# Performance work log

Hardware: AMD Instinct MI355X
Metric: run time of the kernel (lower is better)

The kernel has to match this reference:

```python
import jax, jax.numpy as jnp
import numpy as np

H = 64  # LSTM hidden size (from LSTM(64, ...))

def _lstm(xs, W, U, b, return_sequences):
    """Keras-convention LSTM. xs: [B, T, D]; W: [D, 4H]; U: [H, 4H]; b: [4H].
    Gate order i, f, g(candidate), o; sigmoid recurrent activation, tanh activation."""
    B = xs.shape[0]
    h_dim = U.shape[0]
    # Precompute input projection for all timesteps (hoists the big GEMM out of scan)
    xW = jnp.einsum('btd,dk->btk', xs, W) + b  # [B, T, 4H]

    def step(carry, xw_t):
        h, c = carry
        z = xw_t + h @ U  # [B, 4H]
        i, f, g, o = jnp.split(z, 4, axis=-1)
        i = jax.nn.sigmoid(i)
        f = jax.nn.sigmoid(f)
        g = jnp.tanh(g)
        o = jax.nn.sigmoid(o)
        c = f * c + i * g
        h = o * jnp.tanh(c)
        return (h, c), h

    h0 = jnp.zeros((B, h_dim), xs.dtype)
    (hT, _), hs = jax.lax.scan(step, (h0, h0), jnp.swapaxes(xW, 0, 1))
    if return_sequences:
        return jnp.swapaxes(hs, 0, 1)  # [B, T, H]
    return hT  # [B, H]


def setup_inputs() -> dict:
    key = jax.random.key(0)
    ks = jax.random.split(key, 17)
    T = 16384
    num_actions = 10
    s = lambda *sh: 1.0 / np.sqrt(sh[0])
    d = {}
    d['x'] = jax.random.normal(ks[0], (T, 2), dtype=jnp.float32)
    # LSTM 1: input dim 2 -> 64
    d['W1'] = jax.random.normal(ks[1], (2, 4 * H), jnp.float32) * s(2)
    d['U1'] = jax.random.normal(ks[2], (H, 4 * H), jnp.float32) * s(H)
    d['b1'] = jnp.concatenate([jnp.zeros(H), jnp.ones(H), jnp.zeros(2 * H)]).astype(jnp.float32)  # unit forget bias
    # LSTM 2: 64 -> 64
    d['W2'] = jax.random.normal(ks[3], (H, 4 * H), jnp.float32) * s(H)
    d['U2'] = jax.random.normal(ks[4], (H, 4 * H), jnp.float32) * s(H)
    d['b2'] = jnp.concatenate([jnp.zeros(H), jnp.ones(H), jnp.zeros(2 * H)]).astype(jnp.float32)
    # LSTM 3: 64 -> 64 (last step only)
    d['W3'] = jax.random.normal(ks[5], (H, 4 * H), jnp.float32) * s(H)
    d['U3'] = jax.random.normal(ks[6], (H, 4 * H), jnp.float32) * s(H)
    d['b3'] = jnp.concatenate([jnp.zeros(H), jnp.ones(H), jnp.zeros(2 * H)]).astype(jnp.float32)
    # Dense heads
    d['Wd1'] = jax.random.normal(ks[7], (H, 20), jnp.float32) * s(H)
    d['bd1'] = jnp.zeros((20,), jnp.float32)
    d['Wd2'] = jax.random.normal(ks[8], (20, 20), jnp.float32) * s(20)
    d['bd2'] = jnp.zeros((20,), jnp.float32)
    d['Wl'] = jax.random.normal(ks[9], (20, num_actions), jnp.float32) * s(20)
    d['bl'] = jnp.zeros((num_actions,), jnp.float32)
    return d


def reference(x, W1, U1, b1, W2, U2, b2, W3, U3, b3, Wd1, bd1, Wd2, bd2, Wl, bl):
    # call(): reshape to [1, -1, 2], cast float32
    xs = jnp.reshape(x.astype(jnp.float32), (1, -1, 2))
    h1 = _lstm(xs, W1, U1, b1, return_sequences=True)   # [1, T, 64]
    h2 = _lstm(h1, W2, U2, b2, return_sequences=True)   # [1, T, 64]
    h3 = _lstm(h2, W3, U3, b3, return_sequences=False)  # [1, 64]
    # Dropout layers are identity at inference (no training=True in call())
    h4 = jax.nn.relu(h3 @ Wd1 + bd1)
    h6 = jax.nn.relu(h4 @ Wd2 + bd2)
    logits = h6 @ Wl + bl  # [1, num_actions]
    return logits
```

## Files before the change

kernel.cpp:

```cpp
#include <hip/hip_runtime.h>

#define H 64
#define G4 256
#define CS 512
#define NC 32
#define PB 16
#define TPB (CS / PB)
#define LOG2E 1.44269504088896f

typedef _Float16 f16x8 __attribute__((ext_vector_type(8)));
typedef float f32x4 __attribute__((ext_vector_type(4)));
typedef __fp16 p16x2 __attribute__((ext_vector_type(2)));

union I4F { int4 i; f16x8 h; };

__device__ __forceinline__ int pack_f16s(float lo, float hi, float sc) {
  union { p16x2 h; int i; } u;
  u.h = __builtin_amdgcn_cvt_pkrtz(lo * sc, hi * sc);
  return u.i;
}
__device__ __forceinline__ void wg_barrier() {
  asm volatile("s_waitcnt lgkmcnt(0)\n\ts_barrier" ::: "memory");
}

__global__ __launch_bounds__(G4) void proj_x(const float* __restrict__ x,
                                             const float* __restrict__ W,
                                             const float* __restrict__ b,
                                             float* __restrict__ xw) {
  const int t = blockIdx.x;
  const int j = threadIdx.x;
  const int G = j >> 6, u = j & 63;
  const float sc = (G == 2) ? 2.f * LOG2E : -LOG2E;
  xw[(size_t)t * G4 + u * 4 + G] =
      sc * fmaf(x[2 * t], W[j], fmaf(x[2 * t + 1], W[G4 + j], b[j]));
}

__global__ __attribute__((amdgpu_flat_work_group_size(G4, G4),
                          amdgpu_waves_per_eu(1, 1)))
void pipe_step(int q, const float* __restrict__ xw1,
               const float* __restrict__ U1, const float* __restrict__ U2,
               const float* __restrict__ U3, const float* __restrict__ W2,
               const float* __restrict__ W3, const float* __restrict__ b2,
               const float* __restrict__ b3, __fp16* __restrict__ h1s,
               __fp16* __restrict__ h2s, __fp16* __restrict__ hb3,
               float* __restrict__ xw2s, float* __restrict__ xw3s,
               float* __restrict__ cst, float* __restrict__ h3out, int T) {
  const int bid = (int)blockIdx.x;
  const int tid = (int)threadIdx.x;

  if (bid >= 3) {
    const int p = bid - 3;
    const int lay = p / PB;
    const int pb = p % PB;
    const int chunk = q - 1 - 2 * lay;
    if (chunk < 0 || chunk >= NC) return;
    const __fp16* hsrc = lay ? h2s : h1s;
    const float* Wm = lay ? W3 : W2;
    const float* bb = lay ? b3 : b2;
    float* dst = (lay ? xw3s : xw2s) + (size_t)(chunk & 1) * CS * G4;
    const int tl0 = pb * TPB;

    __shared__ float sh[TPB * H];
    {
      union { int4 i; __fp16 hh[8]; } uu;
      uu.i = ((const int4*)(hsrc + (size_t)(chunk * CS + tl0) * H))[tid];
      float4 lo = make_float4(uu.hh[0], uu.hh[1], uu.hh[2], uu.hh[3]);
      float4 hi = make_float4(uu.hh[4], uu.hh[5], uu.hh[6], uu.hh[7]);
      ((float4*)sh)[2 * tid] = lo;
      ((float4*)sh)[2 * tid + 1] = hi;
    }
    __syncthreads();

    const int j = tid;
    const int G = j >> 6, u = j & 63;
    const int pos = (u << 2) | G;
    const float scl = (G == 2) ? 2.f * LOG2E : -LOG2E;
    float w[H];
#pragma unroll
    for (int k = 0; k < H; ++k) w[k] = Wm[k * G4 + j];
    const float bj = bb[j];

    for (int tt = 0; tt < TPB; ++tt) {
      const float4* h4 = (const float4*)(sh + tt * H);
      float a0 = bj, a1 = 0.f, a2 = 0.f, a3 = 0.f;
#pragma unroll
      for (int kk = 0; kk < H / 4; ++kk) {
        float4 hv = h4[kk];
        a0 = fmaf(hv.x, w[4 * kk + 0], a0);
        a1 = fmaf(hv.y, w[4 * kk + 1], a1);
        a2 = fmaf(hv.z, w[4 * kk + 2], a2);
        a3 = fmaf(hv.w, w[4 * kk + 3], a3);
      }
      dst[(size_t)(tl0 + tt) * G4 + pos] = scl * ((a0 + a1) + (a2 + a3));
    }
    return;
  }

  const int role = bid;
  const int chunk = q - 2 * role;
  if (chunk < 0 || chunk >= NC) return;
  const int t0 = chunk * CS, t1 = t0 + CS;

  __shared__ int4 sh_h[2][8];

  const int wv = tid >> 6;
  const int n = tid & 15;
  const int kg = (tid & 63) >> 4;
  const int u_own = (wv << 4) | ((n & 3) << 2) | kg;

  const float* U = (role == 0) ? U1 : ((role == 1) ? U2 : U3);
  const float scl = ((n & 3) == 2) ? 2.f * LOG2E : -LOG2E;

  I4F au[4][2];
#pragma unroll
  for (int tau = 0; tau < 4; ++tau) {
    const int colA = ((n & 3) << 6) | (wv << 4) | (tau << 2) | (n >> 2);
#pragma unroll
    for (int kap = 0; kap < 2; ++kap) {
      const int k0 = kap * 32 + kg * 8;
      au[tau][kap].i = make_int4(
          pack_f16s(U[(k0 + 0) * G4 + colA], U[(k0 + 1) * G4 + colA], scl),
          pack_f16s(U[(k0 + 2) * G4 + colA], U[(k0 + 3) * G4 + colA], scl),
          pack_f16s(U[(k0 + 4) * G4 + colA], U[(k0 + 5) * G4 + colA], scl),
          pack_f16s(U[(k0 + 6) * G4 + colA], U[(k0 + 7) * G4 + colA], scl));
      asm volatile("" : "+v"(au[tau][kap].i.x), "+v"(au[tau][kap].i.y),
                       "+v"(au[tau][kap].i.z), "+v"(au[tau][kap].i.w));
    }
  }

  const float* xbase =
      (role == 0) ? (xw1 + (size_t)t0 * G4)
                  : ((role == 1) ? xw2s : xw3s) + (size_t)(chunk & 1) * CS * G4;
  __fp16* hout = (role == 0) ? h1s : h2s;

  float c = (chunk == 0) ? 0.f : cst[role * 64 + u_own];
  if (tid < 8) {
    int4 v = make_int4(0, 0, 0, 0);
    if (chunk > 0) {
      const int4* src = (role == 0)
              ? (const int4*)(h1s + (size_t)(t0 - 1) * H)
              : (role == 1) ? (const int4*)(h2s + (size_t)(t0 - 1) * H)
                            : (const int4*)hb3;
      v = src[tid];
    }
    sh_h[(t0 - 1) & 1][tid] = v;
  }
  wg_barrier();

  float4 nxt = *(const float4*)(xbase + (size_t)0 * G4 + u_own * 4);

  for (int tt = 0; tt < CS; ++tt) {
    const int s = t0 + tt;
    I4F b0, b1;
    b0.i = sh_h[(s - 1) & 1][kg];
    b1.i = sh_h[(s - 1) & 1][4 + kg];

    f32x4 a0 = {0.f, 0.f, 0.f, 0.f}, a1 = a0, a2 = a0, a3 = a0;
    a0 = __builtin_amdgcn_mfma_f32_16x16x32_f16(au[0][0].h, b0.h, a0, 0, 0, 0);
    a1 = __builtin_amdgcn_mfma_f32_16x16x32_f16(au[1][0].h, b0.h, a1, 0, 0, 0);
    a2 = __builtin_amdgcn_mfma_f32_16x16x32_f16(au[2][0].h, b0.h, a2, 0, 0, 0);
    a3 = __builtin_amdgcn_mfma_f32_16x16x32_f16(au[3][0].h, b0.h, a3, 0, 0, 0);
    a0 = __builtin_amdgcn_mfma_f32_16x16x32_f16(au[0][1].h, b1.h, a0, 0, 0, 0);
    a1 = __builtin_amdgcn_mfma_f32_16x16x32_f16(au[1][1].h, b1.h, a1, 0, 0, 0);
    a2 = __builtin_amdgcn_mfma_f32_16x16x32_f16(au[2][1].h, b1.h, a2, 0, 0, 0);
    a3 = __builtin_amdgcn_mfma_f32_16x16x32_f16(au[3][1].h, b1.h, a3, 0, 0, 0);

    const bool se = ((n & 1) == 0);
    const bool s01 = ((n & 2) == 0);
    float z0, z1, z2, z3;
    {
      float lo, hi;
      lo = se ? a0[0] : a1[0]; hi = se ? a2[0] : a3[0]; z0 = s01 ? lo : hi;
      lo = se ? a0[1] : a1[1]; hi = se ? a2[1] : a3[1]; z1 = s01 ? lo : hi;
      lo = se ? a0[2] : a1[2]; hi = se ? a2[2] : a3[2]; z2 = s01 ? lo : hi;
      lo = se ? a0[3] : a1[3]; hi = se ? a2[3] : a3[3]; z3 = s01 ? lo : hi;
    }
    z0 += nxt.x; z1 += nxt.y; z2 += nxt.z; z3 += nxt.w;

    const int tn = (tt + 1 < CS) ? (tt + 1) : tt;
    nxt = *(const float4*)(xbase + (size_t)tn * G4 + u_own * 4);

    const float gi = __builtin_amdgcn_rcpf(1.f + exp2f(z0));
    const float gf = __builtin_amdgcn_rcpf(1.f + exp2f(z1));
    const float gg = fmaf(-2.f, __builtin_amdgcn_rcpf(1.f + exp2f(z2)), 1.f);
    const float go = __builtin_amdgcn_rcpf(1.f + exp2f(z3));
    c = fmaf(gf, c, gi * gg);
    const float th =
        fmaf(-2.f, __builtin_amdgcn_rcpf(1.f + exp2f(c * (2.f * LOG2E))), 1.f);
    const float h = go * th;

    if (n < 4) {
      ((__fp16*)&sh_h[s & 1][0])[u_own] = (__fp16)h;
      if (role < 2) {
        hout[(size_t)s * H + u_own] = (__fp16)h;
      } else {
        if (tt == CS - 1) hb3[u_own] = (__fp16)h;
        if (s == T - 1) h3out[u_own] = h;
      }
      if (tt == CS - 1) cst[role * 64 + u_own] = c;
    }
    wg_barrier();
  }
}

__global__ __launch_bounds__(64) void head_k(const float* __restrict__ hlast,
                                             const float* __restrict__ Wd1,
                                             const float* __restrict__ bd1,
                                             const float* __restrict__ Wd2,
                                             const float* __restrict__ bd2,
                                             const float* __restrict__ Wl,
                                             const float* __restrict__ bl,
                                             float* __restrict__ out) {
  __shared__ float s_h[H];
  __shared__ float s_a[20];
  __shared__ float s_b[20];
  const int j = threadIdx.x;
  s_h[j] = hlast[j];
  __syncthreads();
  if (j < 20) {
    float acc = bd1[j];
#pragma unroll
    for (int k = 0; k < H; ++k) acc = fmaf(s_h[k], Wd1[k * 20 + j], acc);
    s_a[j] = fmaxf(acc, 0.f);
  }
  __syncthreads();
  if (j < 20) {
    float acc = bd2[j];
#pragma unroll
    for (int k = 0; k < 20; ++k) acc = fmaf(s_a[k], Wd2[k * 20 + j], acc);
    s_b[j] = fmaxf(acc, 0.f);
  }
  __syncthreads();
  if (j < 10) {
    float acc = bl[j];
#pragma unroll
    for (int k = 0; k < 20; ++k) acc = fmaf(s_b[k], Wl[k * 10 + j], acc);
    out[j] = acc;
  }
}

extern "C" void kernel_launch(void* const* d_in, const int* in_sizes, int n_in,
                              void* d_out, int out_size, void* d_ws, size_t ws_size,
                              hipStream_t stream) {
  const float* x   = (const float*)d_in[0];
  const float* W1  = (const float*)d_in[1];
  const float* U1  = (const float*)d_in[2];
  const float* b1  = (const float*)d_in[3];
  const float* W2  = (const float*)d_in[4];
  const float* U2  = (const float*)d_in[5];
  const float* b2  = (const float*)d_in[6];
  const float* W3  = (const float*)d_in[7];
  const float* U3  = (const float*)d_in[8];
  const float* b3  = (const float*)d_in[9];
  const float* Wd1 = (const float*)d_in[10];
  const float* bd1 = (const float*)d_in[11];
  const float* Wd2 = (const float*)d_in[12];
  const float* bd2 = (const float*)d_in[13];
  const float* Wl  = (const float*)d_in[14];
  const float* bl  = (const float*)d_in[15];
  const int T = in_sizes[0] / 2;

  float* xw1 = (float*)d_ws;
  __fp16* h1s = (__fp16*)(xw1 + (size_t)T * G4);
  __fp16* h2s = h1s + (size_t)T * H;
  float* xw2s = (float*)(h2s + (size_t)T * H);
  float* xw3s = xw2s + 2 * CS * G4;
  __fp16* hb3 = (__fp16*)(xw3s + 2 * CS * G4);
  float* cst = (float*)(hb3 + H);
  float* h3out = cst + 192;

  proj_x<<<T, G4, 0, stream>>>(x, W1, b1, xw1);
  for (int q = 0; q < NC + 4; ++q) {
    pipe_step<<<3 + 2 * PB, G4, 0, stream>>>(q, xw1, U1, U2, U3, W2, W3, b2,
                                             b3, h1s, h2s, hb3, xw2s, xw3s,
                                             cst, h3out, T);
  }
  head_k<<<1, 64, 0, stream>>>(h3out, Wd1, bd1, Wd2, bd2, Wl, bl,
                               (float*)d_out);
}
```

Before: 8.283 ms.

## Run each LSTM recurrence in a single wave using bpermute instead of barriers

The recurrent role blocks now use one 64-lane wave that holds all four column slices of U in registers. Each step issues 32 MFMAs, selects the lane's own result, and rebuilds the B operand with ds_bpermute shuffles, so the per-step LDS write and workgroup barrier are gone. Chunk-boundary hidden state is now carried in an fp32 buffer shared by all roles. This adds 4x the MFMA work and register pressure per wave in exchange for removing inter-wave synchronisation from the serial critical path. The accurate exp2f calls are also replaced with the raw hardware exp2 intrinsic.

After: 10.95 ms. +32.3%, slower.

```diff
diff --git a/kernel.cpp b/kernel.cpp
--- a/kernel.cpp
+++ b/kernel.cpp
@@ -19,8 +19,14 @@
   u.h = __builtin_amdgcn_cvt_pkrtz(lo * sc, hi * sc);
   return u.i;
 }
-__device__ __forceinline__ void wg_barrier() {
-  asm volatile("s_waitcnt lgkmcnt(0)\n\ts_barrier" ::: "memory");
+__device__ __forceinline__ int pack_f16(float lo, float hi) {
+  union { p16x2 h; int i; } u;
+  u.h = __builtin_amdgcn_cvt_pkrtz(lo, hi);
+  return u.i;
+}
+__device__ __forceinline__ float bperm_f(int src_lane, float v) {
+  return __int_as_float(
+      __builtin_amdgcn_ds_bpermute(src_lane << 2, __float_as_int(v)));
 }
 
 __global__ __launch_bounds__(G4) void proj_x(const float* __restrict__ x,
@@ -42,8 +48,8 @@
                const float* __restrict__ U3, const float* __restrict__ W2,
                const float* __restrict__ W3, const float* __restrict__ b2,
                const float* __restrict__ b3, __fp16* __restrict__ h1s,
-               __fp16* __restrict__ h2s, __fp16* __restrict__ hb3,
-               float* __restrict__ xw2s, float* __restrict__ xw3s,
+               __fp16* __restrict__ h2s, float* __restrict__ xw2s,
+               float* __restrict__ xw3s, float* __restrict__ hbnd,
                float* __restrict__ cst, float* __restrict__ h3out, int T) {
   const int bid = (int)blockIdx.x;
   const int tid = (int)threadIdx.x;
@@ -99,32 +105,34 @@
   const int role = bid;
   const int chunk = q - 2 * role;
   if (chunk < 0 || chunk >= NC) return;
-  const int t0 = chunk * CS, t1 = t0 + CS;
-
-  __shared__ int4 sh_h[2][8];
-
-  const int wv = tid >> 6;
+  if (tid >= 64) return;
+  const int t0 = chunk * CS;
+
   const int n = tid & 15;
-  const int kg = (tid & 63) >> 4;
-  const int u_own = (wv << 4) | ((n & 3) << 2) | kg;
+  const int kg = tid >> 4;
+  const int grp = n >> 2;
+  const int u_own = 4 * n + kg;
 
   const float* U = (role == 0) ? U1 : ((role == 1) ? U2 : U3);
   const float scl = ((n & 3) == 2) ? 2.f * LOG2E : -LOG2E;
 
-  I4F au[4][2];
-#pragma unroll
-  for (int tau = 0; tau < 4; ++tau) {
-    const int colA = ((n & 3) << 6) | (wv << 4) | (tau << 2) | (n >> 2);
-#pragma unroll
-    for (int kap = 0; kap < 2; ++kap) {
-      const int k0 = kap * 32 + kg * 8;
-      au[tau][kap].i = make_int4(
-          pack_f16s(U[(k0 + 0) * G4 + colA], U[(k0 + 1) * G4 + colA], scl),
-          pack_f16s(U[(k0 + 2) * G4 + colA], U[(k0 + 3) * G4 + colA], scl),
-          pack_f16s(U[(k0 + 4) * G4 + colA], U[(k0 + 5) * G4 + colA], scl),
-          pack_f16s(U[(k0 + 6) * G4 + colA], U[(k0 + 7) * G4 + colA], scl));
-      asm volatile("" : "+v"(au[tau][kap].i.x), "+v"(au[tau][kap].i.y),
-                       "+v"(au[tau][kap].i.z), "+v"(au[tau][kap].i.w));
+  I4F au[4][4][2];
+#pragma unroll
+  for (int w = 0; w < 4; ++w) {
+#pragma unroll
+    for (int tau = 0; tau < 4; ++tau) {
+      const int colA = ((n & 3) << 6) | (w << 4) | (tau << 2) | grp;
+#pragma unroll
+      for (int kap = 0; kap < 2; ++kap) {
+        const int k0 = kap * 32 + kg * 8;
+        au[w][tau][kap].i = make_int4(
+            pack_f16s(U[(k0 + 0) * G4 + colA], U[(k0 + 1) * G4 + colA], scl),
+            pack_f16s(U[(k0 + 2) * G4 + colA], U[(k0 + 3) * G4 + colA], scl),
+            pack_f16s(U[(k0 + 4) * G4 + colA], U[(k0 + 5) * G4 + colA], scl),
+            pack_f16s(U[(k0 + 6) * G4 + colA], U[(k0 + 7) * G4 + colA], scl));
+        asm volatile("" : "+v"(au[w][tau][kap].i.x), "+v"(au[w][tau][kap].i.y),
+                         "+v"(au[w][tau][kap].i.z), "+v"(au[w][tau][kap].i.w));
+      }
     }
   }
 
@@ -133,73 +141,106 @@
                   : ((role == 1) ? xw2s : xw3s) + (size_t)(chunk & 1) * CS * G4;
   __fp16* hout = (role == 0) ? h1s : h2s;
 
-  float c = (chunk == 0) ? 0.f : cst[role * 64 + u_own];
-  if (tid < 8) {
-    int4 v = make_int4(0, 0, 0, 0);
-    if (chunk > 0) {
-      const int4* src = (role == 0)
-              ? (const int4*)(h1s + (size_t)(t0 - 1) * H)
-              : (role == 1) ? (const int4*)(h2s + (size_t)(t0 - 1) * H)
-                            : (const int4*)hb3;
-      v = src[tid];
-    }
-    sh_h[(t0 - 1) & 1][tid] = v;
-  }
-  wg_barrier();
+  float c;
+  I4F bf0, bf1;
+  if (chunk == 0) {
+    c = 0.f;
+    bf0.i = make_int4(0, 0, 0, 0);
+    bf1.i = make_int4(0, 0, 0, 0);
+  } else {
+    c = cst[role * 64 + u_own];
+    const float* hb = hbnd + role * 64;
+    float4 lo = *(const float4*)(hb + 8 * kg);
+    float4 hi = *(const float4*)(hb + 8 * kg + 4);
+    bf0.i = make_int4(pack_f16(lo.x, lo.y), pack_f16(lo.z, lo.w),
+                      pack_f16(hi.x, hi.y), pack_f16(hi.z, hi.w));
+    float4 lo1 = *(const float4*)(hb + 32 + 8 * kg);
+    float4 hi1 = *(const float4*)(hb + 32 + 8 * kg + 4);
+    bf1.i = make_int4(pack_f16(lo1.x, lo1.y), pack_f16(lo1.z, lo1.w),
+                      pack_f16(hi1.x, hi1.y), pack_f16(hi1.z, hi1.w));
+  }
+
+  f32x4 zero4 = {0.f, 0.f, 0.f, 0.f};
+  asm volatile("" : "+v"(zero4));
 
   float4 nxt = *(const float4*)(xbase + (size_t)0 * G4 + u_own * 4);
+  const int b2k = 2 * kg;
 
   for (int tt = 0; tt < CS; ++tt) {
-    const int s = t0 + tt;
-    I4F b0, b1;
-    b0.i = sh_h[(s - 1) & 1][kg];
-    b1.i = sh_h[(s - 1) & 1][4 + kg];
-
-    f32x4 a0 = {0.f, 0.f, 0.f, 0.f}, a1 = a0, a2 = a0, a3 = a0;
-    a0 = __builtin_amdgcn_mfma_f32_16x16x32_f16(au[0][0].h, b0.h, a0, 0, 0, 0);
-    a1 = __builtin_amdgcn_mfma_f32_16x16x32_f16(au[1][0].h, b0.h, a1, 0, 0, 0);
-    a2 = __builtin_amdgcn_mfma_f32_16x16x32_f16(au[2][0].h, b0.h, a2, 0, 0, 0);
-    a3 = __builtin_amdgcn_mfma_f32_16x16x32_f16(au[3][0].h, b0.h, a3, 0, 0, 0);
-    a0 = __builtin_amdgcn_mfma_f32_16x16x32_f16(au[0][1].h, b1.h, a0, 0, 0, 0);
-    a1 = __builtin_amdgcn_mfma_f32_16x16x32_f16(au[1][1].h, b1.h, a1, 0, 0, 0);
-    a2 = __builtin_amdgcn_mfma_f32_16x16x32_f16(au[2][1].h, b1.h, a2, 0, 0, 0);
-    a3 = __builtin_amdgcn_mfma_f32_16x16x32_f16(au[3][1].h, b1.h, a3, 0, 0, 0);
-
-    const bool se = ((n & 1) == 0);
-    const bool s01 = ((n & 2) == 0);
     float z0, z1, z2, z3;
-    {
-      float lo, hi;
-      lo = se ? a0[0] : a1[0]; hi = se ? a2[0] : a3[0]; z0 = s01 ? lo : hi;
-      lo = se ? a0[1] : a1[1]; hi = se ? a2[1] : a3[1]; z1 = s01 ? lo : hi;
-      lo = se ? a0[2] : a1[2]; hi = se ? a2[2] : a3[2]; z2 = s01 ? lo : hi;
-      lo = se ? a0[3] : a1[3]; hi = se ? a2[3] : a3[3]; z3 = s01 ? lo : hi;
+#pragma unroll
+    for (int w = 0; w < 4; ++w) {
+      f32x4 a0, a1, a2, a3;
+      a0 = __builtin_amdgcn_mfma_f32_16x16x32_f16(au[w][0][0].h, bf0.h, zero4, 0, 0, 0);
+      a1 = __builtin_amdgcn_mfma_f32_16x16x32_f16(au[w][1][0].h, bf0.h, zero4, 0, 0, 0);
+      a2 = __builtin_amdgcn_mfma_f32_16x16x32_f16(au[w][2][0].h, bf0.h, zero4, 0, 0, 0);
+      a3 = __builtin_amdgcn_mfma_f32_16x16x32_f16(au[w][3][0].h, bf0.h, zero4, 0, 0, 0);
+      a0 = __builtin_amdgcn_mfma_f32_16x16x32_f16(au[w][0][1].h, bf1.h, a0, 0, 0, 0);
+      a1 = __builtin_amdgcn_mfma_f32_16x16x32_f16(au[w][1][1].h, bf1.h, a1, 0, 0, 0);
+      a2 = __builtin_amdgcn_mfma_f32_16x16x32_f16(au[w][2][1].h, bf1.h, a2, 0, 0, 0);
+      a3 = __builtin_amdgcn_mfma_f32_16x16x32_f16(au[w][3][1].h, bf1.h, a3, 0, 0, 0);
+
+      const bool se = ((n & 1) == 0);
+      const bool s01 = ((n & 2) == 0);
+      float s0, s1, s2, s3;
+      {
+        float lo, hi;
+        lo = se ? a0[0] : a1[0]; hi = se ? a2[0] : a3[0]; s0 = s01 ? lo : hi;
+        lo = se ? a0[1] : a1[1]; hi = se ? a2[1] : a3[1]; s1 = s01 ? lo : hi;
+        lo = se ? a0[2] : a1[2]; hi = se ? a2[2] : a3[2]; s2 = s01 ? lo : hi;
+        lo = se ? a0[3] : a1[3]; hi = se ? a2[3] : a3[3]; s3 = s01 ? lo : hi;
+      }
+      if (w == 0) {
+        z0 = s0; z1 = s1; z2 = s2; z3 = s3;
+      } else {
+        const bool gs = (grp == w);
+        z0 = gs ? s0 : z0; z1 = gs ? s1 : z1;
+        z2 = gs ? s2 : z2; z3 = gs ? s3 : z3;
+      }
     }
     z0 += nxt.x; z1 += nxt.y; z2 += nxt.z; z3 += nxt.w;
 
     const int tn = (tt + 1 < CS) ? (tt + 1) : tt;
     nxt = *(const float4*)(xbase + (size_t)tn * G4 + u_own * 4);
 
-    const float gi = __builtin_amdgcn_rcpf(1.f + exp2f(z0));
-    const float gf = __builtin_amdgcn_rcpf(1.f + exp2f(z1));
-    const float gg = fmaf(-2.f, __builtin_amdgcn_rcpf(1.f + exp2f(z2)), 1.f);
-    const float go = __builtin_amdgcn_rcpf(1.f + exp2f(z3));
+    const float gi = __builtin_amdgcn_rcpf(1.f + __builtin_amdgcn_exp2f(z0));
+    const float gf = __builtin_amdgcn_rcpf(1.f + __builtin_amdgcn_exp2f(z1));
+    const float gg =
+        fmaf(-2.f, __builtin_amdgcn_rcpf(1.f + __builtin_amdgcn_exp2f(z2)), 1.f);
+    const float go = __builtin_amdgcn_rcpf(1.f + __builtin_amdgcn_exp2f(z3));
     c = fmaf(gf, c, gi * gg);
-    const float th =
-        fmaf(-2.f, __builtin_amdgcn_rcpf(1.f + exp2f(c * (2.f * LOG2E))), 1.f);
+    const float th = fmaf(
+        -2.f,
+        __builtin_amdgcn_rcpf(1.f + __builtin_amdgcn_exp2f(c * (2.f * LOG2E))),
+        1.f);
     const float h = go * th;
 
-    if (n < 4) {
-      ((__fp16*)&sh_h[s & 1][0])[u_own] = (__fp16)h;
-      if (role < 2) {
-        hout[(size_t)s * H + u_own] = (__fp16)h;
-      } else {
-        if (tt == CS - 1) hb3[u_own] = (__fp16)h;
-        if (s == T - 1) h3out[u_own] = h;
-      }
-      if (tt == CS - 1) cst[role * 64 + u_own] = c;
-    }
-    wg_barrier();
+    const int s = t0 + tt;
+    if (role < 2) {
+      hout[(size_t)s * H + u_own] = (__fp16)h;
+    } else if (s == T - 1) {
+      h3out[u_own] = h;
+    }
+
+    {
+      const float q0 = bperm_f(b2k + 0, h),  q1 = bperm_f(b2k + 16, h);
+      const float q2 = bperm_f(b2k + 32, h), q3 = bperm_f(b2k + 48, h);
+      const float q4 = bperm_f(b2k + 1, h),  q5 = bperm_f(b2k + 17, h);
+      const float q6 = bperm_f(b2k + 33, h), q7 = bperm_f(b2k + 49, h);
+      bf0.i = make_int4(pack_f16(q0, q1), pack_f16(q2, q3),
+                        pack_f16(q4, q5), pack_f16(q6, q7));
+      const float r0 = bperm_f(b2k + 8, h),  r1 = bperm_f(b2k + 24, h);
+      const float r2 = bperm_f(b2k + 40, h), r3 = bperm_f(b2k + 56, h);
+      const float r4 = bperm_f(b2k + 9, h),  r5 = bperm_f(b2k + 25, h);
+      const float r6 = bperm_f(b2k + 41, h), r7 = bperm_f(b2k + 57, h);
+      bf1.i = make_int4(pack_f16(r0, r1), pack_f16(r2, r3),
+                        pack_f16(r4, r5), pack_f16(r6, r7));
+    }
+
+    if (tt == CS - 1) {
+      cst[role * 64 + u_own] = c;
+      hbnd[role * 64 + u_own] = h;
+    }
   }
 }
 
@@ -265,14 +306,14 @@
   __fp16* h2s = h1s + (size_t)T * H;
   float* xw2s = (float*)(h2s + (size_t)T * H);
   float* xw3s = xw2s + 2 * CS * G4;
-  __fp16* hb3 = (__fp16*)(xw3s + 2 * CS * G4);
-  float* cst = (float*)(hb3 + H);
+  float* hbnd = xw3s + 2 * CS * G4;
+  float* cst = hbnd + 192;
   float* h3out = cst + 192;
 
   proj_x<<<T, G4, 0, stream>>>(x, W1, b1, xw1);
   for (int q = 0; q < NC + 4; ++q) {
     pipe_step<<<3 + 2 * PB, G4, 0, stream>>>(q, xw1, U1, U2, U3, W2, W3, b2,
-                                             b3, h1s, h2s, hb3, xw2s, xw3s,
+                                             b3, h1s, h2s, xw2s, xw3s, hbnd,
                                              cst, h3out, T);
   }
   head_k<<<1, 64, 0, stream>>>(h3out, Wd1, bd1, Wd2, bd2, Wl, bl,
```
